# Kernel tuning notes

Hardware: AMD Instinct MI355X
Metric: run time of the kernel (lower is better)

The kernel has to match this reference:

```python
import jax, jax.numpy as jnp
import numpy as np

NEG = -1.0e9  # masked_fill value from the original module

def setup_inputs() -> dict:
    key = jax.random.key(0)
    kq, kk, kv, km = jax.random.split(key, 4)
    B, H, S, D = 4, 16, 2048, 64
    Q = jax.random.normal(kq, (B, H, S, D), dtype=jnp.float32)
    K = jax.random.normal(kk, (B, H, S, D), dtype=jnp.float32)
    V = jax.random.normal(kv, (B, H, S, D), dtype=jnp.float32)
    # boolean mask, True = masked out (broadcast over batch and heads)
    mask = jax.random.randint(km, (1, 1, S, S), 0, 2).astype(jnp.bool_)
    return {"Q": Q, "K": K, "V": V, "mask": mask}

def reference(Q, K, V, mask):
    d_k = K.shape[-1]
    scale = 1.0 / jnp.sqrt(jnp.asarray(d_k, dtype=Q.dtype))
    # [B,H,S,S] attention scores
    scores = jnp.einsum("bhqd,bhkd->bhqk", Q, K) * scale
    scores = jnp.where(mask, jnp.asarray(NEG, dtype=scores.dtype), scores)
    weights = jax.nn.softmax(scores, axis=-1)
    # dropout is identity in eval mode (self.training == False)
    return jnp.einsum("bhqk,bhkd->bhqd", weights, V)
```

## Files before the change

### kernel.cpp

```cpp
#include <hip/hip_runtime.h>
#include <stdint.h>

#define SQ 2048
#define DH 64

typedef __attribute__((ext_vector_type(8))) short bf16x8;
typedef __attribute__((ext_vector_type(4))) short bf16x4;
typedef __attribute__((ext_vector_type(4))) float f32x4;

static __device__ __forceinline__ unsigned short f2bf_rne(float x) {
  union { float f; uint32_t u; } v; v.f = x;
  uint32_t u = v.u;
  return (unsigned short)((u + 0x7FFFu + ((u >> 16) & 1u)) >> 16);
}

static __device__ __forceinline__ uint32_t pack_hi(float a, float b) {
  uint32_t au = __float_as_uint(a), bu = __float_as_uint(b);
#if __has_builtin(__builtin_amdgcn_perm)
  return __builtin_amdgcn_perm(bu, au, 0x07060302u);
#else
  return (bu & 0xFFFF0000u) | (au >> 16);
#endif
}

static __device__ __forceinline__ uint32_t pack_sel(float a, float b, uint32_t sel) {
#if __has_builtin(__builtin_amdgcn_perm)
  return __builtin_amdgcn_perm(__float_as_uint(b), __float_as_uint(a), sel);
#else
  uint32_t r = 0;
  uint64_t src = ((uint64_t)__float_as_uint(b) << 32) | __float_as_uint(a);
  for (int i = 0; i < 4; ++i) {
    uint32_t sb = (sel >> (8 * i)) & 0xFF;
    uint32_t byte = (sb < 8) ? (uint32_t)((src >> (8 * sb)) & 0xFF) : 0u;
    r |= byte << (8 * i);
  }
  return r;
#endif
}

static __device__ __forceinline__ float fast_exp2(float x) {
#if __has_builtin(__builtin_amdgcn_exp2f)
  return __builtin_amdgcn_exp2f(x);
#else
  return exp2f(x);
#endif
}

#if __has_builtin(__builtin_amdgcn_mfma_f32_16x16x16_bf16)
#define MFMA_PV(a, b, c) __builtin_amdgcn_mfma_f32_16x16x16_bf16((a), (b), (c), 0, 0, 0)
#else
#define MFMA_PV(a, b, c) __builtin_amdgcn_mfma_f32_16x16x16bf16_1k((a), (b), (c), 0, 0, 0)
#endif

typedef __attribute__((address_space(1))) const void as1_const_void;
typedef __attribute__((address_space(3))) void as3_void;
static __device__ __forceinline__ void gload_lds16(const void* g, void* l, int lane) {
#if __has_builtin(__builtin_amdgcn_global_load_lds)
  __builtin_amdgcn_global_load_lds((as1_const_void*)g, (as3_void*)l, 16, 0, 0);
#else
  *(uint4*)((char*)l + lane * 16) = *(const uint4*)g;
#endif
}

__global__ __launch_bounds__(256) void pack_all(const float* __restrict__ K,
                                                const float* __restrict__ V,
                                                const int* __restrict__ mask,
                                                uint4* __restrict__ pk,
                                                uint2* __restrict__ pv,
                                                uint2* __restrict__ pm) {
  const int t = threadIdx.x;
  if (blockIdx.x < 2048) {
    __shared__ uint32_t Vw[64][33];
    const int bt = blockIdx.x;
    {
      const float* src = K + (size_t)bt * 64 * DH;
      uint4* dst = pk + (size_t)bt * 512;
#pragma unroll
      for (int j = 0; j < 2; ++j) {
        int i = t + j * 256;
        int kk = i >> 3, cp = i & 7;
        int c = cp ^ (kk & 7);
        const float4* s4 = (const float4*)(src + (size_t)kk * DH + c * 8);
        float4 a = s4[0], b = s4[1];
        uint4 w;
        w.x = pack_hi(a.x, a.y); w.y = pack_hi(a.z, a.w);
        w.z = pack_hi(b.x, b.y); w.w = pack_hi(b.z, b.w);
        dst[i] = w;
      }
    }
    {
      const float* src = V + (size_t)bt * 64 * DH;
#pragma unroll
      for (int half = 0; half < 2; ++half) {
        int kp = (t >> 4) + half * 16;
        int d4 = (t & 15) * 4;
        float4 a = *(const float4*)(src + (size_t)(2 * kp) * DH + d4);
        float4 b = *(const float4*)(src + (size_t)(2 * kp + 1) * DH + d4);
        Vw[d4 + 0][kp] = pack_hi(a.x, b.x);
        Vw[d4 + 1][kp] = pack_hi(a.y, b.y);
        Vw[d4 + 2][kp] = pack_hi(a.z, b.z);
        Vw[d4 + 3][kp] = pack_hi(a.w, b.w);
      }
      __syncthreads();
      uint2* dst = pv + (size_t)bt * 1024;
#pragma unroll
      for (int j = 0; j < 4; ++j) {
        int o = t + j * 256;
        int d = o >> 4, up = o & 15;
        int u = up ^ (d & 15);
        uint2 w;
        w.x = Vw[d][2 * u]; w.y = Vw[d][2 * u + 1];
        dst[o] = w;
      }
    }
  } else {
    __shared__ uint2 Lm[16][17];
    const int bid = blockIdx.x - 2048;
    const int qb = bid >> 5, gb = bid & 31;
    {
      int qq = t >> 4, gg = t & 15;
      int4 m = *(const int4*)(mask + (size_t)(qb * 16 + qq) * SQ + (gb * 64 + gg * 4));
      uint2 w;
      w.x = (m.x ? 0x00000C0Cu : 0x00000302u) | (m.y ? 0x0C0C0000u : 0x07060000u);
      w.y = (m.z ? 0x00000C0Cu : 0x00000302u) | (m.w ? 0x0C0C0000u : 0x07060000u);
      Lm[gg][qq] = w;
    }
    __syncthreads();
    {
      int gg = t >> 4, qq = t & 15;
      pm[(size_t)(gb * 16 + gg) * 2048 + qb * 16 + qq] = Lm[gg][qq];
    }
  }
}

__global__ void pack_mask_kernel(const int* __restrict__ mask,
                                 unsigned long long* __restrict__ bits) {
  const int lane = threadIdx.x & 63;
  const int gw = (blockIdx.x * blockDim.x + threadIdx.x) >> 6;
  const int nw = (gridDim.x * blockDim.x) >> 6;
  for (int w = gw; w < SQ * SQ / 64; w += nw) {
    int v = mask[(size_t)w * 64 + lane];
    unsigned long long b = __ballot(v != 0);
    if (lane == 0) bits[(size_t)(w & 31) * SQ + (w >> 5)] = b;
  }
}

__global__ __launch_bounds__(256, 4) void attn3(
    const uint4* __restrict__ pk, const uint4* __restrict__ pv,
    const uint2* __restrict__ pm, const float* __restrict__ Qg,
    float* __restrict__ Og) {
  __shared__ __align__(16) uint8_t smem[32768];

  const int id = blockIdx.x;
  const int bh = id & 63;
  const int qblk = id >> 6;
  const int t = threadIdx.x;
  const int wave = t >> 6, lane = t & 63, col = lane & 15, quad = lane >> 4;

  const float* Qb = Qg + (size_t)bh * SQ * DH;
  float* Ob = Og + (size_t)bh * SQ * DH;
  const uint4* pkb = pk + (size_t)bh * 32 * 512;
  const uint4* pvb = pv + (size_t)bh * 32 * 512;
  const int q0 = qblk * 128 + wave * 32;

  const float QSCALE = 0.18033688011112042f;
  bf16x8 qf[2][2];
#pragma unroll
  for (int s = 0; s < 2; ++s) {
    int q = q0 + s * 16 + col;
#pragma unroll
    for (int j = 0; j < 2; ++j) {
      const float4* p = (const float4*)(Qb + (size_t)q * DH + j * 32 + quad * 8);
      float4 a = p[0], b = p[1];
      bf16x8 f;
      f[0] = (short)f2bf_rne(a.x * QSCALE); f[1] = (short)f2bf_rne(a.y * QSCALE);
      f[2] = (short)f2bf_rne(a.z * QSCALE); f[3] = (short)f2bf_rne(a.w * QSCALE);
      f[4] = (short)f2bf_rne(b.x * QSCALE); f[5] = (short)f2bf_rne(b.y * QSCALE);
      f[6] = (short)f2bf_rne(b.z * QSCALE); f[7] = (short)f2bf_rne(b.w * QSCALE);
      qf[s][j] = f;
    }
  }

  const unsigned ka0 = col * 128 + ((quad ^ (col & 7)) * 16);
  const unsigned ka1 = col * 128 + (((4 + quad) ^ (col & 7)) * 16);
  unsigned va[4];
#pragma unroll
  for (int kt = 0; kt < 4; ++kt)
    va[kt] = 16384u + col * 128 + (((kt * 4 + quad) ^ col) * 8);
  const char* pmt = (const char*)pm + (size_t)(quad * 2048 + q0 + col) * 8;

  f32x4 acc[2][4];
  f32x4 accl[2];
#pragma unroll
  for (int s = 0; s < 2; ++s) {
#pragma unroll
    for (int dt = 0; dt < 4; ++dt)
#pragma unroll
      for (int r = 0; r < 4; ++r) acc[s][dt][r] = 0.0f;
#pragma unroll
    for (int r = 0; r < 4; ++r) accl[s][r] = 0.0f;
  }
  bf16x4 vones;
  vones[0] = (short)0x3F80; vones[1] = (short)0x3F80;
  vones[2] = (short)0x3F80; vones[3] = (short)0x3F80;
  const f32x4 fz = {0.0f, 0.0f, 0.0f, 0.0f};

  gload_lds16(pkb + t,       smem + wave * 1024,         lane);
  gload_lds16(pkb + t + 256, smem + 4096 + wave * 1024,  lane);
  gload_lds16(pvb + t,       smem + 16384 + wave * 1024, lane);
  gload_lds16(pvb + t + 256, smem + 20480 + wave * 1024, lane);
  unsigned buf = 0;

  for (int tile = 0; tile < 32; ++tile) {
    __syncthreads();
    const int tn = (tile < 31) ? tile + 1 : 31;
    const unsigned ob = buf ^ 8192u;

    const uint4* pkt = pkb + (size_t)tn * 512;
    const uint4* pvt = pvb + (size_t)tn * 512;
    gload_lds16(pkt + t,       smem + ob + wave * 1024,         lane);
    gload_lds16(pkt + t + 256, smem + ob + 4096 + wave * 1024,  lane);
    gload_lds16(pvt + t,       smem + ob + 16384 + wave * 1024, lane);
    gload_lds16(pvt + t + 256, smem + ob + 20480 + wave * 1024, lane);

#pragma unroll
    for (int kt = 0; kt < 4; ++kt) {
      const bf16x8 kf0 = *(const bf16x8*)(smem + buf + kt * 2048 + ka0);
      const bf16x8 kf1 = *(const bf16x8*)(smem + buf + kt * 2048 + ka1);
      uint2 mw[2];
#pragma unroll
      for (int s = 0; s < 2; ++s)
        mw[s] = *(const uint2*)(pmt + (size_t)kt * 65536 + s * 128);

      uint32_t pf[2][2];
#pragma unroll
      for (int s = 0; s < 2; ++s) {
        f32x4 st = __builtin_amdgcn_mfma_f32_16x16x32_bf16(kf0, qf[s][0], fz, 0, 0, 0);
        st = __builtin_amdgcn_mfma_f32_16x16x32_bf16(kf1, qf[s][1], st, 0, 0, 0);
        float p0 = fast_exp2(st[0]), p1 = fast_exp2(st[1]);
        float p2 = fast_exp2(st[2]), p3 = fast_exp2(st[3]);
        pf[s][0] = pack_sel(p0, p1, mw[s].x);
        pf[s][1] = pack_sel(p2, p3, mw[s].y);
      }

      union { uint32_t u[2]; bf16x4 v; } pw0, pw1;
      pw0.u[0] = pf[0][0]; pw0.u[1] = pf[0][1];
      pw1.u[0] = pf[1][0]; pw1.u[1] = pf[1][1];
      accl[0] = MFMA_PV(vones, pw0.v, accl[0]);
      accl[1] = MFMA_PV(vones, pw1.v, accl[1]);
#pragma unroll
      for (int dt = 0; dt < 4; ++dt) {
        union { uint2 u2; bf16x4 v; } vf;
        vf.u2 = *(const uint2*)(smem + buf + va[kt] + dt * 2048);
        acc[0][dt] = MFMA_PV(vf.v, pw0.v, acc[0][dt]);
        acc[1][dt] = MFMA_PV(vf.v, pw1.v, acc[1][dt]);
      }
    }

    buf = ob;
    pmt += 262144;
  }

#pragma unroll
  for (int s = 0; s < 2; ++s) {
    float inv = 1.0f / accl[s][0];
    int q = q0 + s * 16 + col;
    float* orow = Ob + (size_t)q * DH;
#pragma unroll
    for (int dt = 0; dt < 4; ++dt) {
      float4 o;
      o.x = acc[s][dt][0] * inv;
      o.y = acc[s][dt][1] * inv;
      o.z = acc[s][dt][2] * inv;
      o.w = acc[s][dt][3] * inv;
      *(float4*)(orow + dt * 16 + quad * 4) = o;
    }
  }
}

__global__ __launch_bounds__(512, 4) void attn_fb(
    const float* __restrict__ Qg, const float* __restrict__ Kg,
    const float* __restrict__ Vg, const unsigned long long* __restrict__ mbits,
    const int* __restrict__ mraw, float* __restrict__ Og) {
  __shared__ __align__(16) unsigned short Klds[2][64][72];
  __shared__ __align__(16) uint32_t Vtlds[2][64][36];
  const int id = blockIdx.x;
  const int bh = id & 63;
  const int qblk = id >> 6;
  const int t = threadIdx.x;
  const int wave = t >> 6, lane = t & 63, col = lane & 15, quad = lane >> 4;
  const float* Qb = Qg + (size_t)bh * SQ * DH;
  const float* Kb = Kg + (size_t)bh * SQ * DH;
  const float* Vb = Vg + (size_t)bh * SQ * DH;
  float* Ob = Og + (size_t)bh * SQ * DH;
  const int q0 = qblk * 256 + wave * 32;
  const int skk = t >> 3, sd8 = (t & 7) * 8, skp = t >> 4, sd4 = (t & 15) * 4;
  const float QSCALE = 0.18033688011112042f;
  bf16x8 qf[2][2];
#pragma unroll
  for (int s = 0; s < 2; ++s) {
    int q = q0 + s * 16 + col;
#pragma unroll
    for (int j = 0; j < 2; ++j) {
      const float4* p = (const float4*)(Qb + (size_t)q * DH + j * 32 + quad * 8);
      float4 a = p[0], b = p[1];
      bf16x8 f;
      f[0] = (short)f2bf_rne(a.x * QSCALE); f[1] = (short)f2bf_rne(a.y * QSCALE);
      f[2] = (short)f2bf_rne(a.z * QSCALE); f[3] = (short)f2bf_rne(a.w * QSCALE);
      f[4] = (short)f2bf_rne(b.x * QSCALE); f[5] = (short)f2bf_rne(b.y * QSCALE);
      f[6] = (short)f2bf_rne(b.z * QSCALE); f[7] = (short)f2bf_rne(b.w * QSCALE);
      qf[s][j] = f;
    }
  }
  f32x4 acc[2][4]; f32x4 accl[2];
#pragma unroll
  for (int s = 0; s < 2; ++s) {
#pragma unroll
    for (int dt = 0; dt < 4; ++dt)
#pragma unroll
      for (int r = 0; r < 4; ++r) acc[s][dt][r] = 0.0f;
#pragma unroll
    for (int r = 0; r < 4; ++r) accl[s][r] = 0.0f;
  }
  bf16x4 vones;
  vones[0] = (short)0x3F80; vones[1] = (short)0x3F80;
  vones[2] = (short)0x3F80; vones[3] = (short)0x3F80;
  const f32x4 fz = {0.0f, 0.0f, 0.0f, 0.0f};
  auto load_mask = [&](int ti, unsigned long long m[2]) {
    if (mbits) {
#pragma unroll
      for (int s = 0; s < 2; ++s)
        m[s] = mbits[(size_t)ti * SQ + (q0 + s * 16 + col)];
    } else {
#pragma unroll
      for (int s = 0; s < 2; ++s) {
        int q = q0 + s * 16 + col;
        unsigned long long mm = 0;
#pragma unroll
        for (int j = 0; j < 4; ++j) {
          int4 mi = *(const int4*)(mraw + (size_t)q * SQ + ti * 64 + j * 16 + quad * 4);
          unsigned long long nib = (unsigned long long)((mi.x != 0) | ((mi.y != 0) << 1) |
                                                        ((mi.z != 0) << 2) | ((mi.w != 0) << 3));
          mm |= nib << (j * 16 + quad * 4);
        }
        m[s] = mm;
      }
    }
  };
  {
    const float4* kp = (const float4*)(Kb + (size_t)skk * DH + sd8);
    float4 k0 = kp[0], k1 = kp[1];
    const float* va = Vb + (size_t)(skp * 2) * DH + sd4;
    float4 v0 = *(const float4*)va, v1 = *(const float4*)(va + DH);
    uint4 kw;
    kw.x = pack_hi(k0.x, k0.y); kw.y = pack_hi(k0.z, k0.w);
    kw.z = pack_hi(k1.x, k1.y); kw.w = pack_hi(k1.z, k1.w);
    *(uint4*)&Klds[0][skk][sd8] = kw;
    Vtlds[0][sd4 + 0][skp] = pack_hi(v0.x, v1.x);
    Vtlds[0][sd4 + 1][skp] = pack_hi(v0.y, v1.y);
    Vtlds[0][sd4 + 2][skp] = pack_hi(v0.z, v1.z);
    Vtlds[0][sd4 + 3][skp] = pack_hi(v0.w, v1.w);
  }
  unsigned long long mcur[2];
  load_mask(0, mcur);
  for (int tile = 0; tile < 32; ++tile) {
    __syncthreads();
    const int cb = tile & 1, nb = cb ^ 1;
    const int tn = (tile + 1 < 32) ? tile + 1 : tile;
    const int kkn = tn * 64;
    const float4* kp = (const float4*)(Kb + (size_t)(kkn + skk) * DH + sd8);
    float4 k0 = kp[0], k1 = kp[1];
    const float* va = Vb + (size_t)(kkn + skp * 2) * DH + sd4;
    float4 v0 = *(const float4*)va;
    float4 v1 = *(const float4*)(va + DH);
    unsigned long long mnxt[2];
    load_mask(tn, mnxt);
    uint32_t pfw[2][4][2];
#pragma unroll
    for (int kt = 0; kt < 4; ++kt) {
      const bf16x8 kf0 = *(const bf16x8*)&Klds[cb][kt * 16 + col][quad * 8];
      const bf16x8 kf1 = *(const bf16x8*)&Klds[cb][kt * 16 + col][32 + quad * 8];
#pragma unroll
      for (int s = 0; s < 2; ++s) {
        f32x4 st = __builtin_amdgcn_mfma_f32_16x16x32_bf16(kf0, qf[s][0], fz, 0, 0, 0);
        st = __builtin_amdgcn_mfma_f32_16x16x32_bf16(kf1, qf[s][1], st, 0, 0, 0);
        uint32_t nib = (uint32_t)(mcur[s] >> (kt * 16 + quad * 4)) & 0xFu;
        float p[4];
#pragma unroll
        for (int r = 0; r < 4; ++r)
          p[r] = fast_exp2(((nib >> r) & 1u) ? -1.0e9f : st[r]);
        pfw[s][kt][0] = pack_hi(p[0], p[1]);
        pfw[s][kt][1] = pack_hi(p[2], p[3]);
      }
    }
    {
      uint4 kw;
      kw.x = pack_hi(k0.x, k0.y); kw.y = pack_hi(k0.z, k0.w);
      kw.z = pack_hi(k1.x, k1.y); kw.w = pack_hi(k1.z, k1.w);
      *(uint4*)&Klds[nb][skk][sd8] = kw;
      Vtlds[nb][sd4 + 0][skp] = pack_hi(v0.x, v1.x);
      Vtlds[nb][sd4 + 1][skp] = pack_hi(v0.y, v1.y);
      Vtlds[nb][sd4 + 2][skp] = pack_hi(v0.z, v1.z);
      Vtlds[nb][sd4 + 3][skp] = pack_hi(v0.w, v1.w);
    }
    mcur[0] = mnxt[0]; mcur[1] = mnxt[1];
#pragma unroll
    for (int kt = 0; kt < 4; ++kt) {
      union { uint32_t u[2]; bf16x4 v; } p0, p1;
      p0.u[0] = pfw[0][kt][0]; p0.u[1] = pfw[0][kt][1];
      p1.u[0] = pfw[1][kt][0]; p1.u[1] = pfw[1][kt][1];
      accl[0] = MFMA_PV(vones, p0.v, accl[0]);
      accl[1] = MFMA_PV(vones, p1.v, accl[1]);
#pragma unroll
      for (int dt = 0; dt < 4; ++dt) {
        union { uint2 u2; bf16x4 v; } cv;
        cv.u2 = *(const uint2*)&Vtlds[cb][dt * 16 + col][kt * 8 + quad * 2];
        acc[0][dt] = MFMA_PV(cv.v, p0.v, acc[0][dt]);
        acc[1][dt] = MFMA_PV(cv.v, p1.v, acc[1][dt]);
      }
    }
  }
#pragma unroll
  for (int s = 0; s < 2; ++s) {
    float inv = 1.0f / accl[s][0];
    int q = q0 + s * 16 + col;
    float* orow = Ob + (size_t)q * DH;
#pragma unroll
    for (int dt = 0; dt < 4; ++dt) {
      float4 o;
      o.x = acc[s][dt][0] * inv;
      o.y = acc[s][dt][1] * inv;
      o.z = acc[s][dt][2] * inv;
      o.w = acc[s][dt][3] * inv;
      *(float4*)(orow + dt * 16 + quad * 4) = o;
    }
  }
}

extern "C" void kernel_launch(void* const* d_in, const int* in_sizes, int n_in,
                              void* d_out, int out_size, void* d_ws, size_t ws_size,
                              hipStream_t stream) {
  const float* Q = (const float*)d_in[0];
  const float* K = (const float*)d_in[1];
  const float* V = (const float*)d_in[2];
  const int* mask = (const int*)d_in[3];
  float* out = (float*)d_out;

  const size_t PK_BYTES = (size_t)64 * 32 * 8192;
  const size_t PV_BYTES = (size_t)64 * 32 * 8192;
  const size_t PM_BYTES = (size_t)512 * 2048 * 8;
  const size_t NEED = PK_BYTES + PV_BYTES + PM_BYTES;

  if (ws_size >= NEED) {
    uint4* pk = (uint4*)d_ws;
    uint2* pv = (uint2*)((char*)d_ws + PK_BYTES);
    uint2* pm = (uint2*)((char*)d_ws + PK_BYTES + PV_BYTES);
    pack_all<<<6144, 256, 0, stream>>>(K, V, mask, pk, pv, pm);
    attn3<<<1024, 256, 0, stream>>>(pk, (uint4*)pv, pm, Q, out);
  } else if (ws_size >= (size_t)SQ * SQ / 8) {
    unsigned long long* bits = (unsigned long long*)d_ws;
    pack_mask_kernel<<<1024, 256, 0, stream>>>(mask, bits);
    attn_fb<<<512, 512, 0, stream>>>(Q, K, V, bits, mask, out);
  } else {
    attn_fb<<<512, 512, 0, stream>>>(Q, K, V, nullptr, mask, out);
  }
}
```

Baseline: 239.9 us.

## Fuse K/V bf16 packing into attention kernel and split mask packing

Removes the separate pack_all pre-pass that wrote bf16 K/V to workspace. The attention kernel now loads fp32 K/V directly, converts them in registers and writes them swizzled into the double-buffered LDS, with the next tile's global loads issued before the compute loop. Mask packing becomes a ballot bitmask kernel followed by an expansion kernel. The row sum is now accumulated in VALU with cross-lane shuffles instead of an MFMA against a ones vector, and s_setprio is raised around the PV MFMAs. The trade is more per-block conversion work and register pressure in exchange for less global traffic and one fewer pass over K/V.

```diff
diff --git a/kernel.cpp b/kernel.cpp
--- a/kernel.cpp
+++ b/kernel.cpp
@@ -38,6 +38,13 @@
 #endif
 }
 
+static __device__ __forceinline__ float bf_lo(uint32_t w) {
+  return __uint_as_float(w << 16);
+}
+static __device__ __forceinline__ float bf_hi(uint32_t w) {
+  return __uint_as_float(w & 0xFFFF0000u);
+}
+
 static __device__ __forceinline__ float fast_exp2(float x) {
 #if __has_builtin(__builtin_amdgcn_exp2f)
   return __builtin_amdgcn_exp2f(x);
@@ -46,92 +53,22 @@
 #endif
 }
 
+static __device__ __forceinline__ void setprio_hi() {
+#if __has_builtin(__builtin_amdgcn_s_setprio)
+  __builtin_amdgcn_s_setprio(1);
+#endif
+}
+static __device__ __forceinline__ void setprio_lo() {
+#if __has_builtin(__builtin_amdgcn_s_setprio)
+  __builtin_amdgcn_s_setprio(0);
+#endif
+}
+
 #if __has_builtin(__builtin_amdgcn_mfma_f32_16x16x16_bf16)
 #define MFMA_PV(a, b, c) __builtin_amdgcn_mfma_f32_16x16x16_bf16((a), (b), (c), 0, 0, 0)
 #else
 #define MFMA_PV(a, b, c) __builtin_amdgcn_mfma_f32_16x16x16bf16_1k((a), (b), (c), 0, 0, 0)
 #endif
-
-typedef __attribute__((address_space(1))) const void as1_const_void;
-typedef __attribute__((address_space(3))) void as3_void;
-static __device__ __forceinline__ void gload_lds16(const void* g, void* l, int lane) {
-#if __has_builtin(__builtin_amdgcn_global_load_lds)
-  __builtin_amdgcn_global_load_lds((as1_const_void*)g, (as3_void*)l, 16, 0, 0);
-#else
-  *(uint4*)((char*)l + lane * 16) = *(const uint4*)g;
-#endif
-}
-
-__global__ __launch_bounds__(256) void pack_all(const float* __restrict__ K,
-                                                const float* __restrict__ V,
-                                                const int* __restrict__ mask,
-                                                uint4* __restrict__ pk,
-                                                uint2* __restrict__ pv,
-                                                uint2* __restrict__ pm) {
-  const int t = threadIdx.x;
-  if (blockIdx.x < 2048) {
-    __shared__ uint32_t Vw[64][33];
-    const int bt = blockIdx.x;
-    {
-      const float* src = K + (size_t)bt * 64 * DH;
-      uint4* dst = pk + (size_t)bt * 512;
-#pragma unroll
-      for (int j = 0; j < 2; ++j) {
-        int i = t + j * 256;
-        int kk = i >> 3, cp = i & 7;
-        int c = cp ^ (kk & 7);
-        const float4* s4 = (const float4*)(src + (size_t)kk * DH + c * 8);
-        float4 a = s4[0], b = s4[1];
-        uint4 w;
-        w.x = pack_hi(a.x, a.y); w.y = pack_hi(a.z, a.w);
-        w.z = pack_hi(b.x, b.y); w.w = pack_hi(b.z, b.w);
-        dst[i] = w;
-      }
-    }
-    {
-      const float* src = V + (size_t)bt * 64 * DH;
-#pragma unroll
-      for (int half = 0; half < 2; ++half) {
-        int kp = (t >> 4) + half * 16;
-        int d4 = (t & 15) * 4;
-        float4 a = *(const float4*)(src + (size_t)(2 * kp) * DH + d4);
-        float4 b = *(const float4*)(src + (size_t)(2 * kp + 1) * DH + d4);
-        Vw[d4 + 0][kp] = pack_hi(a.x, b.x);
-        Vw[d4 + 1][kp] = pack_hi(a.y, b.y);
-        Vw[d4 + 2][kp] = pack_hi(a.z, b.z);
-        Vw[d4 + 3][kp] = pack_hi(a.w, b.w);
-      }
-      __syncthreads();
-      uint2* dst = pv + (size_t)bt * 1024;
-#pragma unroll
-      for (int j = 0; j < 4; ++j) {
-        int o = t + j * 256;
-        int d = o >> 4, up = o & 15;
-        int u = up ^ (d & 15);
-        uint2 w;
-        w.x = Vw[d][2 * u]; w.y = Vw[d][2 * u + 1];
-        dst[o] = w;
-      }
-    }
-  } else {
-    __shared__ uint2 Lm[16][17];
-    const int bid = blockIdx.x - 2048;
-    const int qb = bid >> 5, gb = bid & 31;
-    {
-      int qq = t >> 4, gg = t & 15;
-      int4 m = *(const int4*)(mask + (size_t)(qb * 16 + qq) * SQ + (gb * 64 + gg * 4));
-      uint2 w;
-      w.x = (m.x ? 0x00000C0Cu : 0x00000302u) | (m.y ? 0x0C0C0000u : 0x07060000u);
-      w.y = (m.z ? 0x00000C0Cu : 0x00000302u) | (m.w ? 0x0C0C0000u : 0x07060000u);
-      Lm[gg][qq] = w;
-    }
-    __syncthreads();
-    {
-      int gg = t >> 4, qq = t & 15;
-      pm[(size_t)(gb * 16 + gg) * 2048 + qb * 16 + qq] = Lm[gg][qq];
-    }
-  }
-}
 
 __global__ void pack_mask_kernel(const int* __restrict__ mask,
                                  unsigned long long* __restrict__ bits) {
@@ -145,9 +82,30 @@
   }
 }
 
-__global__ __launch_bounds__(256, 4) void attn3(
-    const uint4* __restrict__ pk, const uint4* __restrict__ pv,
-    const uint2* __restrict__ pm, const float* __restrict__ Qg,
+__global__ __launch_bounds__(256) void pm_expand(
+    const unsigned long long* __restrict__ bits, uint2* __restrict__ pm) {
+  const int t = threadIdx.x;
+  const int tile = blockIdx.x >> 3;
+  const int q = (blockIdx.x & 7) * 256 + t;
+  const unsigned long long m = bits[(size_t)tile * SQ + q];
+#pragma unroll
+  for (int kt = 0; kt < 4; ++kt) {
+#pragma unroll
+    for (int quad = 0; quad < 4; ++quad) {
+      uint32_t nib = (uint32_t)(m >> (kt * 16 + quad * 4)) & 0xFu;
+      uint2 w;
+      w.x = ((nib & 1u) ? 0x00000C0Cu : 0x00000302u) |
+            ((nib & 2u) ? 0x0C0C0000u : 0x07060000u);
+      w.y = ((nib & 4u) ? 0x00000C0Cu : 0x00000302u) |
+            ((nib & 8u) ? 0x0C0C0000u : 0x07060000u);
+      pm[(size_t)(tile * 16 + kt * 4 + quad) * SQ + q] = w;
+    }
+  }
+}
+
+__global__ __launch_bounds__(256, 4) void attn4(
+    const float* __restrict__ Qg, const float* __restrict__ Kg,
+    const float* __restrict__ Vg, const uint2* __restrict__ pm,
     float* __restrict__ Og) {
   __shared__ __align__(16) uint8_t smem[32768];
 
@@ -158,9 +116,9 @@
   const int wave = t >> 6, lane = t & 63, col = lane & 15, quad = lane >> 4;
 
   const float* Qb = Qg + (size_t)bh * SQ * DH;
+  const float* Kb = Kg + (size_t)bh * SQ * DH;
+  const float* Vb = Vg + (size_t)bh * SQ * DH;
   float* Ob = Og + (size_t)bh * SQ * DH;
-  const uint4* pkb = pk + (size_t)bh * 32 * 512;
-  const uint4* pvb = pv + (size_t)bh * 32 * 512;
   const int q0 = qblk * 128 + wave * 32;
 
   const float QSCALE = 0.18033688011112042f;
@@ -181,6 +139,28 @@
     }
   }
 
+  const int kk0 = t >> 3;
+  const int kc = (t & 7) ^ (kk0 & 7);
+  const float* kp0 = Kb + (size_t)kk0 * DH + kc * 8;
+  const float* kp1 = kp0 + (size_t)32 * DH;
+  const unsigned wK0 = (unsigned)t * 16u;
+  const unsigned wK1 = wK0 + 4096u;
+  const int vkp = t >> 4;
+  const int vd4 = (t & 15) * 4;
+  const float* vp0 = Vb + (size_t)(2 * vkp) * DH + vd4;
+  const float* vp1 = vp0 + (size_t)32 * DH;
+  unsigned voff[2][4];
+#pragma unroll
+  for (int h = 0; h < 2; ++h) {
+    int kp = vkp + h * 16;
+#pragma unroll
+    for (int j = 0; j < 4; ++j) {
+      int d = vd4 + j;
+      int o = d * 16 + ((kp >> 1) ^ (d & 15));
+      voff[h][j] = (unsigned)(o * 8 + (kp & 1) * 4) + 16384u;
+    }
+  }
+
   const unsigned ka0 = col * 128 + ((quad ^ (col & 7)) * 16);
   const unsigned ka1 = col * 128 + (((4 + quad) ^ (col & 7)) * 16);
   unsigned va[4];
@@ -190,38 +170,50 @@
   const char* pmt = (const char*)pm + (size_t)(quad * 2048 + q0 + col) * 8;
 
   f32x4 acc[2][4];
-  f32x4 accl[2];
-#pragma unroll
-  for (int s = 0; s < 2; ++s) {
+  float lsum[2] = {0.0f, 0.0f};
+#pragma unroll
+  for (int s = 0; s < 2; ++s)
 #pragma unroll
     for (int dt = 0; dt < 4; ++dt)
 #pragma unroll
       for (int r = 0; r < 4; ++r) acc[s][dt][r] = 0.0f;
-#pragma unroll
-    for (int r = 0; r < 4; ++r) accl[s][r] = 0.0f;
-  }
-  bf16x4 vones;
-  vones[0] = (short)0x3F80; vones[1] = (short)0x3F80;
-  vones[2] = (short)0x3F80; vones[3] = (short)0x3F80;
   const f32x4 fz = {0.0f, 0.0f, 0.0f, 0.0f};
 
-  gload_lds16(pkb + t,       smem + wave * 1024,         lane);
-  gload_lds16(pkb + t + 256, smem + 4096 + wave * 1024,  lane);
-  gload_lds16(pvb + t,       smem + 16384 + wave * 1024, lane);
-  gload_lds16(pvb + t + 256, smem + 20480 + wave * 1024, lane);
+  {
+    float4 a0 = ((const float4*)kp0)[0], b0 = ((const float4*)kp0)[1];
+    float4 a1 = ((const float4*)kp1)[0], b1 = ((const float4*)kp1)[1];
+    uint4 w0, w1;
+    w0.x = pack_hi(a0.x, a0.y); w0.y = pack_hi(a0.z, a0.w);
+    w0.z = pack_hi(b0.x, b0.y); w0.w = pack_hi(b0.z, b0.w);
+    w1.x = pack_hi(a1.x, a1.y); w1.y = pack_hi(a1.z, a1.w);
+    w1.z = pack_hi(b1.x, b1.y); w1.w = pack_hi(b1.z, b1.w);
+    *(uint4*)(smem + wK0) = w0;
+    *(uint4*)(smem + wK1) = w1;
+    float4 va0 = ((const float4*)vp0)[0], vb0 = *(const float4*)(vp0 + DH);
+    float4 va1 = ((const float4*)vp1)[0], vb1 = *(const float4*)(vp1 + DH);
+    *(uint32_t*)(smem + voff[0][0]) = pack_hi(va0.x, vb0.x);
+    *(uint32_t*)(smem + voff[0][1]) = pack_hi(va0.y, vb0.y);
+    *(uint32_t*)(smem + voff[0][2]) = pack_hi(va0.z, vb0.z);
+    *(uint32_t*)(smem + voff[0][3]) = pack_hi(va0.w, vb0.w);
+    *(uint32_t*)(smem + voff[1][0]) = pack_hi(va1.x, vb1.x);
+    *(uint32_t*)(smem + voff[1][1]) = pack_hi(va1.y, vb1.y);
+    *(uint32_t*)(smem + voff[1][2]) = pack_hi(va1.z, vb1.z);
+    *(uint32_t*)(smem + voff[1][3]) = pack_hi(va1.w, vb1.w);
+  }
   unsigned buf = 0;
 
   for (int tile = 0; tile < 32; ++tile) {
     __syncthreads();
-    const int tn = (tile < 31) ? tile + 1 : 31;
     const unsigned ob = buf ^ 8192u;
 
-    const uint4* pkt = pkb + (size_t)tn * 512;
-    const uint4* pvt = pvb + (size_t)tn * 512;
-    gload_lds16(pkt + t,       smem + ob + wave * 1024,         lane);
-    gload_lds16(pkt + t + 256, smem + ob + 4096 + wave * 1024,  lane);
-    gload_lds16(pvt + t,       smem + ob + 16384 + wave * 1024, lane);
-    gload_lds16(pvt + t + 256, smem + ob + 20480 + wave * 1024, lane);
+    float4 ka0f, kb0f, ka1f, kb1f, va0, vb0, va1, vb1;
+    if (tile < 31) {
+      kp0 += 64 * DH; kp1 += 64 * DH; vp0 += 64 * DH; vp1 += 64 * DH;
+      ka0f = ((const float4*)kp0)[0]; kb0f = ((const float4*)kp0)[1];
+      ka1f = ((const float4*)kp1)[0]; kb1f = ((const float4*)kp1)[1];
+      va0 = ((const float4*)vp0)[0]; vb0 = *(const float4*)(vp0 + DH);
+      va1 = ((const float4*)vp1)[0]; vb1 = *(const float4*)(vp1 + DH);
+    }
 
 #pragma unroll
     for (int kt = 0; kt < 4; ++kt) {
@@ -241,20 +233,42 @@
         float p2 = fast_exp2(st[2]), p3 = fast_exp2(st[3]);
         pf[s][0] = pack_sel(p0, p1, mw[s].x);
         pf[s][1] = pack_sel(p2, p3, mw[s].y);
+        lsum[s] += (bf_lo(pf[s][0]) + bf_hi(pf[s][0])) +
+                   (bf_lo(pf[s][1]) + bf_hi(pf[s][1]));
       }
 
+      union { uint2 u2; bf16x4 v; } vf[4];
+#pragma unroll
+      for (int dt = 0; dt < 4; ++dt)
+        vf[dt].u2 = *(const uint2*)(smem + buf + va[kt] + dt * 2048);
       union { uint32_t u[2]; bf16x4 v; } pw0, pw1;
       pw0.u[0] = pf[0][0]; pw0.u[1] = pf[0][1];
       pw1.u[0] = pf[1][0]; pw1.u[1] = pf[1][1];
-      accl[0] = MFMA_PV(vones, pw0.v, accl[0]);
-      accl[1] = MFMA_PV(vones, pw1.v, accl[1]);
+      setprio_hi();
 #pragma unroll
       for (int dt = 0; dt < 4; ++dt) {
-        union { uint2 u2; bf16x4 v; } vf;
-        vf.u2 = *(const uint2*)(smem + buf + va[kt] + dt * 2048);
-        acc[0][dt] = MFMA_PV(vf.v, pw0.v, acc[0][dt]);
-        acc[1][dt] = MFMA_PV(vf.v, pw1.v, acc[1][dt]);
+        acc[0][dt] = MFMA_PV(vf[dt].v, pw0.v, acc[0][dt]);
+        acc[1][dt] = MFMA_PV(vf[dt].v, pw1.v, acc[1][dt]);
       }
+      setprio_lo();
+    }
+
+    if (tile < 31) {
+      uint4 w0, w1;
+      w0.x = pack_hi(ka0f.x, ka0f.y); w0.y = pack_hi(ka0f.z, ka0f.w);
+      w0.z = pack_hi(kb0f.x, kb0f.y); w0.w = pack_hi(kb0f.z, kb0f.w);
+      w1.x = pack_hi(ka1f.x, ka1f.y); w1.y = pack_hi(ka1f.z, ka1f.w);
+      w1.z = pack_hi(kb1f.x, kb1f.y); w1.w = pack_hi(kb1f.z, kb1f.w);
+      *(uint4*)(smem + ob + wK0) = w0;
+      *(uint4*)(smem + ob + wK1) = w1;
+      *(uint32_t*)(smem + ob + voff[0][0]) = pack_hi(va0.x, vb0.x);
+      *(uint32_t*)(smem + ob + voff[0][1]) = pack_hi(va0.y, vb0.y);
+      *(uint32_t*)(smem + ob + voff[0][2]) = pack_hi(va0.z, vb0.z);
+      *(uint32_t*)(smem + ob + voff[0][3]) = pack_hi(va0.w, vb0.w);
+      *(uint32_t*)(smem + ob + voff[1][0]) = pack_hi(va1.x, vb1.x);
+      *(uint32_t*)(smem + ob + voff[1][1]) = pack_hi(va1.y, vb1.y);
+      *(uint32_t*)(smem + ob + voff[1][2]) = pack_hi(va1.z, vb1.z);
+      *(uint32_t*)(smem + ob + voff[1][3]) = pack_hi(va1.w, vb1.w);
     }
 
     buf = ob;
@@ -263,7 +277,10 @@
 
 #pragma unroll
   for (int s = 0; s < 2; ++s) {
-    float inv = 1.0f / accl[s][0];
+    float l = lsum[s];
+    l += __shfl_xor(l, 16);
+    l += __shfl_xor(l, 32);
+    float inv = 1.0f / l;
     int q = q0 + s * 16 + col;
     float* orow = Ob + (size_t)q * DH;
 #pragma unroll
@@ -446,18 +463,17 @@
   const int* mask = (const int*)d_in[3];
   float* out = (float*)d_out;
 
-  const size_t PK_BYTES = (size_t)64 * 32 * 8192;
-  const size_t PV_BYTES = (size_t)64 * 32 * 8192;
   const size_t PM_BYTES = (size_t)512 * 2048 * 8;
-  const size_t NEED = PK_BYTES + PV_BYTES + PM_BYTES;
+  const size_t BITS_BYTES = (size_t)SQ * SQ / 8;
+  const size_t NEED = PM_BYTES + BITS_BYTES;
 
   if (ws_size >= NEED) {
-    uint4* pk = (uint4*)d_ws;
-    uint2* pv = (uint2*)((char*)d_ws + PK_BYTES);
-    uint2* pm = (uint2*)((char*)d_ws + PK_BYTES + PV_BYTES);
-    pack_all<<<6144, 256, 0, stream>>>(K, V, mask, pk, pv, pm);
-    attn3<<<1024, 256, 0, stream>>>(pk, (uint4*)pv, pm, Q, out);
-  } else if (ws_size >= (size_t)SQ * SQ / 8) {
+    uint2* pm = (uint2*)d_ws;
+    unsigned long long* bits = (unsigned long long*)((char*)d_ws + PM_BYTES);
+    pack_mask_kernel<<<1024, 256, 0, stream>>>(mask, bits);
+    pm_expand<<<256, 256, 0, stream>>>(bits, pm);
+    attn4<<<1024, 256, 0, stream>>>(Q, K, V, pm, out);
+  } else if (ws_size >= BITS_BYTES) {
     unsigned long long* bits = (unsigned long long*)d_ws;
     pack_mask_kernel<<<1024, 256, 0, stream>>>(mask, bits);
     attn_fb<<<512, 512, 0, stream>>>(Q, K, V, bits, mask, out);
```

New measurement: 297.4 us. 1.24x slower.

## Give each wave a private K/V double buffer, dropping block-wide barriers

Applied to the files above, without the earlier changes.

Each wave now streams its own 16-key K/V sub-tile into a private LDS double buffer over 128 iterations, so the per-tile __syncthreads is gone and a manual vmcnt wait orders the loads instead. The V packing layout loses its XOR swizzle to suit the new linear per-wave reads. Mask words are prefetched one iteration ahead, and s_setprio raises priority around the PV MFMAs. The cost is that every wave reloads the same K/V data, which multiplies global and L2 traffic by the wave count. The unswizzled V layout may also cause LDS bank conflicts.

```diff
diff --git a/kernel.cpp b/kernel.cpp
--- a/kernel.cpp
+++ b/kernel.cpp
@@ -46,6 +46,23 @@
 #endif
 }
 
+static __device__ __forceinline__ void setprio_hi() {
+#if __has_builtin(__builtin_amdgcn_s_setprio)
+  __builtin_amdgcn_s_setprio(1);
+#endif
+}
+static __device__ __forceinline__ void setprio_lo() {
+#if __has_builtin(__builtin_amdgcn_s_setprio)
+  __builtin_amdgcn_s_setprio(0);
+#endif
+}
+
+static __device__ __forceinline__ void sched_barrier0() {
+#if __has_builtin(__builtin_amdgcn_sched_barrier)
+  __builtin_amdgcn_sched_barrier(0);
+#endif
+}
+
 #if __has_builtin(__builtin_amdgcn_mfma_f32_16x16x16_bf16)
 #define MFMA_PV(a, b, c) __builtin_amdgcn_mfma_f32_16x16x16_bf16((a), (b), (c), 0, 0, 0)
 #else
@@ -106,8 +123,7 @@
 #pragma unroll
       for (int j = 0; j < 4; ++j) {
         int o = t + j * 256;
-        int d = o >> 4, up = o & 15;
-        int u = up ^ (d & 15);
+        int u = o >> 6, d = o & 63;
         uint2 w;
         w.x = Vw[d][2 * u]; w.y = Vw[d][2 * u + 1];
         dst[o] = w;
@@ -145,7 +161,7 @@
   }
 }
 
-__global__ __launch_bounds__(256, 4) void attn3(
+__global__ __launch_bounds__(256, 4) void attn5(
     const uint4* __restrict__ pk, const uint4* __restrict__ pv,
     const uint2* __restrict__ pm, const float* __restrict__ Qg,
     float* __restrict__ Og) {
@@ -159,8 +175,8 @@
 
   const float* Qb = Qg + (size_t)bh * SQ * DH;
   float* Ob = Og + (size_t)bh * SQ * DH;
-  const uint4* pkb = pk + (size_t)bh * 32 * 512;
-  const uint4* pvb = pv + (size_t)bh * 32 * 512;
+  const char* pkb = (const char*)(pk + (size_t)bh * 32 * 512);
+  const char* pvb = (const char*)(pv + (size_t)bh * 32 * 512);
   const int q0 = qblk * 128 + wave * 32;
 
   const float QSCALE = 0.18033688011112042f;
@@ -181,12 +197,10 @@
     }
   }
 
+  const unsigned wb = (unsigned)wave * 8192u;
   const unsigned ka0 = col * 128 + ((quad ^ (col & 7)) * 16);
   const unsigned ka1 = col * 128 + (((4 + quad) ^ (col & 7)) * 16);
-  unsigned va[4];
-#pragma unroll
-  for (int kt = 0; kt < 4; ++kt)
-    va[kt] = 16384u + col * 128 + (((kt * 4 + quad) ^ col) * 8);
+  const unsigned vb0 = 2048u + quad * 512u + col * 8u;
   const char* pmt = (const char*)pm + (size_t)(quad * 2048 + q0 + col) * 8;
 
   f32x4 acc[2][4];
@@ -205,60 +219,67 @@
   vones[2] = (short)0x3F80; vones[3] = (short)0x3F80;
   const f32x4 fz = {0.0f, 0.0f, 0.0f, 0.0f};
 
-  gload_lds16(pkb + t,       smem + wave * 1024,         lane);
-  gload_lds16(pkb + t + 256, smem + 4096 + wave * 1024,  lane);
-  gload_lds16(pvb + t,       smem + 16384 + wave * 1024, lane);
-  gload_lds16(pvb + t + 256, smem + 20480 + wave * 1024, lane);
-  unsigned buf = 0;
-
-  for (int tile = 0; tile < 32; ++tile) {
-    __syncthreads();
-    const int tn = (tile < 31) ? tile + 1 : 31;
-    const unsigned ob = buf ^ 8192u;
-
-    const uint4* pkt = pkb + (size_t)tn * 512;
-    const uint4* pvt = pvb + (size_t)tn * 512;
-    gload_lds16(pkt + t,       smem + ob + wave * 1024,         lane);
-    gload_lds16(pkt + t + 256, smem + ob + 4096 + wave * 1024,  lane);
-    gload_lds16(pvt + t,       smem + ob + 16384 + wave * 1024, lane);
-    gload_lds16(pvt + t + 256, smem + ob + 20480 + wave * 1024, lane);
-
-#pragma unroll
-    for (int kt = 0; kt < 4; ++kt) {
-      const bf16x8 kf0 = *(const bf16x8*)(smem + buf + kt * 2048 + ka0);
-      const bf16x8 kf1 = *(const bf16x8*)(smem + buf + kt * 2048 + ka1);
-      uint2 mw[2];
-#pragma unroll
-      for (int s = 0; s < 2; ++s)
-        mw[s] = *(const uint2*)(pmt + (size_t)kt * 65536 + s * 128);
-
-      uint32_t pf[2][2];
-#pragma unroll
-      for (int s = 0; s < 2; ++s) {
-        f32x4 st = __builtin_amdgcn_mfma_f32_16x16x32_bf16(kf0, qf[s][0], fz, 0, 0, 0);
-        st = __builtin_amdgcn_mfma_f32_16x16x32_bf16(kf1, qf[s][1], st, 0, 0, 0);
-        float p0 = fast_exp2(st[0]), p1 = fast_exp2(st[1]);
-        float p2 = fast_exp2(st[2]), p3 = fast_exp2(st[3]);
-        pf[s][0] = pack_sel(p0, p1, mw[s].x);
-        pf[s][1] = pack_sel(p2, p3, mw[s].y);
-      }
-
-      union { uint32_t u[2]; bf16x4 v; } pw0, pw1;
-      pw0.u[0] = pf[0][0]; pw0.u[1] = pf[0][1];
-      pw1.u[0] = pf[1][0]; pw1.u[1] = pf[1][1];
-      accl[0] = MFMA_PV(vones, pw0.v, accl[0]);
-      accl[1] = MFMA_PV(vones, pw1.v, accl[1]);
-#pragma unroll
-      for (int dt = 0; dt < 4; ++dt) {
-        union { uint2 u2; bf16x4 v; } vf;
-        vf.u2 = *(const uint2*)(smem + buf + va[kt] + dt * 2048);
-        acc[0][dt] = MFMA_PV(vf.v, pw0.v, acc[0][dt]);
-        acc[1][dt] = MFMA_PV(vf.v, pw1.v, acc[1][dt]);
-      }
-    }
-
-    buf = ob;
-    pmt += 262144;
+  gload_lds16(pkb + lane * 16,        smem + wb,        lane);
+  gload_lds16(pkb + 1024 + lane * 16, smem + wb + 1024, lane);
+  gload_lds16(pvb + lane * 16,        smem + wb + 2048, lane);
+  gload_lds16(pvb + 1024 + lane * 16, smem + wb + 3072, lane);
+  uint2 mwc0 = *(const uint2*)(pmt);
+  uint2 mwc1 = *(const uint2*)(pmt + 128);
+  unsigned bo = 0;
+
+#pragma unroll 2
+  for (int it = 0; it < 128; ++it) {
+    const int itn = (it < 127) ? it + 1 : 127;
+    const unsigned ob = bo ^ 4096u;
+
+    sched_barrier0();
+    const char* sk = pkb + (size_t)itn * 2048;
+    const char* sv = pvb + (size_t)itn * 2048;
+    gload_lds16(sk + lane * 16,        smem + wb + ob,        lane);
+    gload_lds16(sk + 1024 + lane * 16, smem + wb + ob + 1024, lane);
+    gload_lds16(sv + lane * 16,        smem + wb + ob + 2048, lane);
+    gload_lds16(sv + 1024 + lane * 16, smem + wb + ob + 3072, lane);
+    const char* pmn = pmt + (size_t)itn * 65536;
+    uint2 mwn0 = *(const uint2*)(pmn);
+    uint2 mwn1 = *(const uint2*)(pmn + 128);
+
+    asm volatile("s_waitcnt vmcnt(6)" ::: "memory");
+    sched_barrier0();
+
+    const bf16x8 kf0 = *(const bf16x8*)(smem + wb + bo + ka0);
+    const bf16x8 kf1 = *(const bf16x8*)(smem + wb + bo + ka1);
+
+    uint32_t pf[2][2];
+    {
+      f32x4 st = __builtin_amdgcn_mfma_f32_16x16x32_bf16(kf0, qf[0][0], fz, 0, 0, 0);
+      st = __builtin_amdgcn_mfma_f32_16x16x32_bf16(kf1, qf[0][1], st, 0, 0, 0);
+      pf[0][0] = pack_sel(fast_exp2(st[0]), fast_exp2(st[1]), mwc0.x);
+      pf[0][1] = pack_sel(fast_exp2(st[2]), fast_exp2(st[3]), mwc0.y);
+    }
+    {
+      f32x4 st = __builtin_amdgcn_mfma_f32_16x16x32_bf16(kf0, qf[1][0], fz, 0, 0, 0);
+      st = __builtin_amdgcn_mfma_f32_16x16x32_bf16(kf1, qf[1][1], st, 0, 0, 0);
+      pf[1][0] = pack_sel(fast_exp2(st[0]), fast_exp2(st[1]), mwc1.x);
+      pf[1][1] = pack_sel(fast_exp2(st[2]), fast_exp2(st[3]), mwc1.y);
+    }
+
+    union { uint32_t u[2]; bf16x4 v; } pw0, pw1;
+    pw0.u[0] = pf[0][0]; pw0.u[1] = pf[0][1];
+    pw1.u[0] = pf[1][0]; pw1.u[1] = pf[1][1];
+    accl[0] = MFMA_PV(vones, pw0.v, accl[0]);
+    accl[1] = MFMA_PV(vones, pw1.v, accl[1]);
+    setprio_hi();
+#pragma unroll
+    for (int dt = 0; dt < 4; ++dt) {
+      union { uint2 u2; bf16x4 v; } vf;
+      vf.u2 = *(const uint2*)(smem + wb + bo + vb0 + dt * 128);
+      acc[0][dt] = MFMA_PV(vf.v, pw0.v, acc[0][dt]);
+      acc[1][dt] = MFMA_PV(vf.v, pw1.v, acc[1][dt]);
+    }
+    setprio_lo();
+
+    mwc0 = mwn0; mwc1 = mwn1;
+    bo = ob;
   }
 
 #pragma unroll
@@ -456,7 +477,7 @@
     uint2* pv = (uint2*)((char*)d_ws + PK_BYTES);
     uint2* pm = (uint2*)((char*)d_ws + PK_BYTES + PV_BYTES);
     pack_all<<<6144, 256, 0, stream>>>(K, V, mask, pk, pv, pm);
-    attn3<<<1024, 256, 0, stream>>>(pk, (uint4*)pv, pm, Q, out);
+    attn5<<<1024, 256, 0, stream>>>(pk, (uint4*)pv, pm, Q, out);
   } else if (ws_size >= (size_t)SQ * SQ / 8) {
     unsigned long long* bits = (unsigned long long*)d_ws;
     pack_mask_kernel<<<1024, 256, 0, stream>>>(mask, bits);
```

Result: slower. 253.4 us (+5.6%).
